# Kernel optimization log

Measured on AMD Instinct MI355X. Metric: run time of the kernel, lower is better.

Reference implementation:

```python
import jax, jax.numpy as jnp
import numpy as np

SCORE_THR = 0.5
RADII = jnp.array([0.5, 0.6, 0.7], dtype=jnp.float32)  # radius_dict[c]; all labels 0..C-1 covered

B, N, C = 2, 8192, 3


def setup_inputs() -> dict:
    key = jax.random.key(0)
    k1, k2 = jax.random.split(key)
    xyz = jax.random.normal(k1, (B, N, 3), dtype=jnp.float32)
    cls_features = jax.random.normal(k2, (B, N, C), dtype=jnp.float32)
    return {"xyz": xyz, "cls_features": cls_features}


def _greedy_select(xyz, cls_features):
    """Greedy per-class radius suppression over the flattened batch.
    Returns sample_idx (B, L) int32, zero-padded exactly like the torch code
    (sample_idx is zeros except slot i of the batch owning selection i)."""
    b, n, _ = xyz.shape
    L = b * n
    scores = jax.nn.sigmoid(jnp.max(cls_features, axis=2))   # (B, N)
    labels = jnp.argmax(cls_features, axis=2)                # (B, N)
    valid = scores >= SCORE_THR

    flat_scores = jnp.where(valid, scores, -jnp.inf).reshape(L)
    order = jnp.argsort(-flat_scores)                        # descending score; invalid sink to end
    sorted_labels = labels.reshape(L)[order]
    sorted_valid = valid.reshape(L)[order]
    sorted_batch = (order // n).astype(jnp.int32)
    sorted_pts = xyz.reshape(L, 3)[order]

    def cond(state):
        i, remaining, _ = state
        return remaining.any() & (i < L)

    def body(state):
        i, remaining, sel_pos = state
        cur = jnp.argmax(remaining)                  # first remaining point in sorted order
        # NB: faithful to the original bug: radius chosen via sorted_labels[i]
        # (loop counter), not the label of the current point.
        r = RADII[sorted_labels[i]]
        d2 = jnp.sum((sorted_pts - sorted_pts[cur]) ** 2, axis=-1)  # (L,)
        suppress = (sorted_batch == sorted_batch[cur]) & (d2 <= r * r)
        return (i + 1, remaining & ~suppress, sel_pos.at[i].set(cur.astype(jnp.int32)))

    sel0 = jnp.full((L,), -1, dtype=jnp.int32)
    _, _, sel_pos = jax.lax.while_loop(cond, body, (jnp.int32(0), sorted_valid, sel0))

    picked = sel_pos >= 0
    orig = jnp.where(picked, order[jnp.maximum(sel_pos, 0)], 0)  # flat index in [0, L)
    bidx = jnp.where(picked, orig // n, 0)
    pidx = jnp.where(picked, orig % n, 0)
    slots = jnp.arange(L)
    # zeros init + scatter exactly mirrors torch: sample_idx[batch, i] = point
    sample_idx = jnp.zeros((b, L), dtype=jnp.int32).at[bidx, slots].set(pidx.astype(jnp.int32))
    return sample_idx


def reference(xyz, cls_features):
    sample_idx = _greedy_select(xyz, cls_features)
    bsz = xyz.shape[0]
    # gather_operation: new_xyz[b, m] = xyz[b, sample_idx[b, m]]
    new_xyz = xyz[jnp.arange(bsz)[:, None], sample_idx]          # (B, L, 3)
    return new_xyz, sample_idx
```

## Files before the change

### kernel.cpp

```cpp
#include <hip/hip_runtime.h>
#include <stdint.h>


#define L_TOT 16384
#define NPT   8192

__device__ __forceinline__ int cellco(float v) {
    int c = (int)floorf((v + 6.4f) * 1.25f);
    return c < 0 ? 0 : (c > 15 ? 15 : c);
}
__device__ __forceinline__ float d2f(float ax, float ay, float az,
                                     float bx, float by, float bz) {
    float dx = __fsub_rn(ax, bx), dy = __fsub_rn(ay, by), dz = __fsub_rn(az, bz);
    return __fadd_rn(__fadd_rn(__fmul_rn(dx, dx), __fmul_rn(dy, dy)), __fmul_rn(dz, dz));
}
__device__ __forceinline__ float rad2(int lb) {
    float rr = (lb == 0) ? 0.5f : ((lb == 1) ? 0.6f : 0.7f);
    return __fmul_rn(rr, rr);
}
__device__ __forceinline__ float rlf(float v, int l) {
    return __uint_as_float(__builtin_amdgcn_readlane(__float_as_uint(v), l));
}
__device__ __forceinline__ int rli(int v, int l) {
    return (int)__builtin_amdgcn_readlane((uint32_t)v, l);
}

__global__ void k1_keys(const float* __restrict__ cls, uint64_t* __restrict__ keys,
                        uint8_t* __restrict__ umeta, uint16_t* __restrict__ sample,
                        int* __restrict__ cellcnt, uint32_t* __restrict__ slab2) {
    int l = blockIdx.x * blockDim.x + threadIdx.x;
    if (l >= L_TOT) return;
    ((uint32_t*)sample)[l] = 0;
    if (l < 8192) cellcnt[l] = 0;
    if (l < 1024) slab2[l] = 0;
    float c0 = cls[l * 3 + 0], c1 = cls[l * 3 + 1], c2 = cls[l * 3 + 2];
    float m = c0; int lab = 0;
    if (c1 > m) { m = c1; lab = 1; }
    if (c2 > m) { m = c2; lab = 2; }
    int valid = (m >= 0.0f) ? 1 : 0;
    float keyf = valid ? m : -__builtin_inff();
    uint32_t u = __float_as_uint(keyf);
    uint32_t o = (u & 0x80000000u) ? ~u : (u | 0x80000000u);
    keys[l] = ((uint64_t)(~o) << 32) | (uint32_t)l;
    umeta[l] = (uint8_t)(lab | (valid << 2));
}

__global__ void __launch_bounds__(256) k2_sort(
    const uint64_t* __restrict__ keys, const uint8_t* __restrict__ umeta,
    const float* __restrict__ xyz,
    float4* __restrict__ spts, uint32_t* __restrict__ slab2, uint16_t* __restrict__ sorder,
    int* __restrict__ cellcnt) {
    __shared__ uint64_t tile[2048];
    __shared__ int psum[256];
    const int t = threadIdx.x;
    const int elem = t & 31, part = t >> 5;
    const int l = blockIdx.x * 32 + elem;
    const uint64_t myk = keys[l];
    int cnt = 0;
    for (int t0 = 0; t0 < L_TOT; t0 += 2048) {
        for (int j = t; j < 2048; j += 256) tile[j] = keys[t0 + j];
        __syncthreads();
        const int b0 = part * 256;
        #pragma unroll 4
        for (int j = 0; j < 256; ++j) cnt += (tile[b0 + j] < myk) ? 1 : 0;
        __syncthreads();
    }
    psum[t] = cnt;
    __syncthreads();
    if (t < 32) {
        int rank = 0;
        #pragma unroll
        for (int q = 0; q < 8; ++q) rank += psum[q * 32 + t];
        const int ll = blockIdx.x * 32 + t;
        int b = ll >> 13, p = ll & (NPT - 1);
        const float* src = xyz + ((size_t)(b * NPT + p)) * 3;
        float x = src[0], y = src[1], z = src[2];
        uint8_t mt = umeta[ll];
        int lab = mt & 3, valid = (mt >> 2) & 1;
        float4 v; v.x = x; v.y = y; v.z = z;
        v.w = __uint_as_float((uint32_t)(b | (valid << 1)));
        spts[rank] = v;
        sorder[rank] = (uint16_t)ll;
        atomicOr(&slab2[rank >> 4], (uint32_t)lab << ((rank & 15) << 1));
        if (valid) {
            int cl = (b << 12) | (cellco(z) << 8) | (cellco(y) << 4) | cellco(x);
            atomicAdd(&cellcnt[cl], 1);
        }
    }
}

__global__ void g2_scan(int* __restrict__ cellcnt, int* __restrict__ cellstart) {
    __shared__ int part[256];
    __shared__ int poff[256];
    int t = threadIdx.x;
    int base = t * 32;
    int loc[32];
    int s = 0;
    for (int k = 0; k < 32; ++k) { loc[k] = cellcnt[base + k]; s += loc[k]; }
    part[t] = s;
    __syncthreads();
    if (t == 0) {
        int run = 0;
        for (int q = 0; q < 256; ++q) { poff[q] = run; run += part[q]; }
    }
    __syncthreads();
    int run = poff[t];
    for (int k = 0; k < 32; ++k) {
        cellstart[base + k] = run; run += loc[k];
        cellcnt[base + k] = 0;
    }
    if (t == 255) cellstart[8192] = run;
}

__global__ void g3_scatter(const float4* __restrict__ spts, const int* __restrict__ cellstart,
                           int* __restrict__ cellfill, float4* __restrict__ cellxyz) {
    int pos = blockIdx.x * blockDim.x + threadIdx.x;
    if (pos >= L_TOT) return;
    float4 v = spts[pos];
    uint32_t w = __float_as_uint(v.w);
    if (!(w & 2u)) return;
    int b = (int)(w & 1u);
    int cl = (b << 12) | (cellco(v.z) << 8) | (cellco(v.y) << 4) | cellco(v.x);
    int slot = atomicAdd(&cellfill[cl], 1);
    float4 o; o.x = v.x; o.y = v.y; o.z = v.z; o.w = __uint_as_float((uint32_t)pos);
    cellxyz[cellstart[cl] + slot] = o;
}

__global__ void __launch_bounds__(1024) k3_greedy(
    const float4* __restrict__ spts, const uint32_t* __restrict__ slab2,
    const uint16_t* __restrict__ sorder,
    const int* __restrict__ cellstart, const float4* __restrict__ cellxyz,
    uint16_t* __restrict__ sample) {
    __shared__ uint64_t qpack[16384];
    __shared__ uint32_t rem[512];
    __shared__ uint32_t alive2[512];
    __shared__ uint16_t cs16[8194];
    __shared__ uint32_t slds2[1024];
    __shared__ float4   pkd[2][128];
    __shared__ int      pkb[2][128];
    __shared__ int      pkn[2];

    const int t = threadIdx.x;
    const int V = cellstart[8192];
    const int NPH = (V + 127) >> 7;

    float4 cv0 = make_float4(0,0,0,0), cv1 = make_float4(0,0,0,0);
    int cord0 = 0, cord1 = 0;
    if (t < 64) {
        cv0 = spts[t]; cv1 = spts[64 + t];
        cord0 = (int)sorder[t]; cord1 = (int)sorder[64 + t];
    }
    for (int j = t; j < 8193; j += 1024) cs16[j] = (uint16_t)cellstart[j];
    for (int j = t; j < 1024; j += 1024) slds2[j] = slab2[j];
    for (int k = t; k < V; k += 1024) {
        float4 q = cellxyz[k];
        int qx = __float2int_rn(__fmul_rn(__fadd_rn(q.x, 8.0f), 4096.0f));
        int qy = __float2int_rn(__fmul_rn(__fadd_rn(q.y, 8.0f), 4096.0f));
        int qz = __float2int_rn(__fmul_rn(__fadd_rn(q.z, 8.0f), 4096.0f));
        qx = qx < 0 ? 0 : (qx > 65535 ? 65535 : qx);
        qy = qy < 0 ? 0 : (qy > 65535 ? 65535 : qy);
        qz = qz < 0 ? 0 : (qz > 65535 ? 65535 : qz);
        uint32_t pos = __float_as_uint(q.w);
        qpack[k] = ((uint64_t)(((uint32_t)qz) | (pos << 16)) << 32)
                 | ((uint32_t)qx | ((uint32_t)qy << 16));
    }
    for (int w = t; w < 512; w += 1024) {
        int lo = w * 32;
        uint32_t m;
        if (V >= lo + 32) m = 0xFFFFFFFFu;
        else if (V <= lo) m = 0u;
        else m = (1u << (V - lo)) - 1u;
        rem[w] = m;
        alive2[w] = m;
    }
    if (t < 2) pkn[t] = 0;
    __syncthreads();

    int ii = 0;
    for (int ph = 0; ph < NPH; ++ph) {
        const int cur = ph & 1, prv = cur ^ 1;
        if (t < 64) {
            const int nb = (ph + 1) << 7;
            int q0 = nb + t;       q0 = q0 > (L_TOT - 1) ? (L_TOT - 1) : q0;
            int q1 = nb + 64 + t;  q1 = q1 > (L_TOT - 1) ? (L_TOT - 1) : q1;
            float4 nv0 = spts[q0], nv1 = spts[q1];
            int nord0 = (int)sorder[q0], nord1 = (int)sorder[q1];

            int o0 = ii + t;      o0 = o0 > (L_TOT - 1) ? (L_TOT - 1) : o0;
            int o1 = ii + 64 + t; o1 = o1 > (L_TOT - 1) ? (L_TOT - 1) : o1;
            float cr0 = rad2((int)((slds2[o0 >> 4] >> ((o0 & 15) << 1)) & 3u));
            float cr1 = rad2((int)((slds2[o1 >> 4] >> ((o1 & 15) << 1)) & 3u));

            const int pos0 = (ph << 7) + t, pos1 = pos0 + 64;
            bool a0 = (pos0 < V) && ((rem[pos0 >> 5] >> (pos0 & 31)) & 1u);
            bool a1 = (pos1 < V) && ((rem[pos1 >> 5] >> (pos1 & 31)) & 1u);
            const int cb0 = cord0 >> 13, cb1 = cord1 >> 13;
            if (__ballot((a0 ? 1 : 0) | (a1 ? 1 : 0))) {
                const int m = pkn[prv];
                for (int j = 0; j < m; ++j) {
                    float4 pk = pkd[prv][j];
                    int pb = pkb[prv][j];
                    if (a0 && cb0 == pb &&
                        d2f(cv0.x, cv0.y, cv0.z, pk.x, pk.y, pk.z) <= pk.w) a0 = false;
                    if (a1 && cb1 == pb &&
                        d2f(cv1.x, cv1.y, cv1.z, pk.x, pk.y, pk.z) <= pk.w) a1 = false;
                }
            }

            int np = 0;
            const int ii0 = ii;
            {
                unsigned long long am = __ballot(a0 ? 1 : 0);
                while (am) {
                    const int jl0 = (int)__builtin_ctzll(am);
                    const unsigned long long am2 = am & (am - 1);
                    const bool has2 = (am2 != 0ull);
                    const int jl1 = has2 ? (int)__builtin_ctzll(am2) : jl0;
                    const float p0x = rlf(cv0.x, jl0), p0y = rlf(cv0.y, jl0), p0z = rlf(cv0.z, jl0);
                    const int   b0  = rli(cord0, jl0) >> 13;
                    const float p1x = rlf(cv0.x, jl1), p1y = rlf(cv0.y, jl1), p1z = rlf(cv0.z, jl1);
                    const int   b1  = rli(cord0, jl1) >> 13;
                    const float r2_0 = rlf((np & 64) ? cr1 : cr0, np & 63);
                    const int np1 = np + 1;
                    const float r2_1 = rlf((np1 & 64) ? cr1 : cr0, np1 & 63);
                    const bool kb = (b0 == b1) &&
                                    (d2f(p1x, p1y, p1z, p0x, p0y, p0z) <= r2_0);
                    const bool two = has2 && !kb;
                    if (t == jl0) {
                        pkd[cur][np] = make_float4(cv0.x, cv0.y, cv0.z, r2_0);
                        pkb[cur][np] = b0;
                        sample[b0 * L_TOT + ii0 + np] = (uint16_t)(cord0 & (NPT - 1));
                    }
                    if (two && t == jl1) {
                        pkd[cur][np1] = make_float4(cv0.x, cv0.y, cv0.z, r2_1);
                        pkb[cur][np1] = b1;
                        sample[b1 * L_TOT + ii0 + np1] = (uint16_t)(cord0 & (NPT - 1));
                    }
                    if (a0) {
                        if (cb0 == b0 && d2f(cv0.x, cv0.y, cv0.z, p0x, p0y, p0z) <= r2_0) a0 = false;
                        if (two && cb0 == b1 && d2f(cv0.x, cv0.y, cv0.z, p1x, p1y, p1z) <= r2_1) a0 = false;
                    }
                    if (a1) {
                        if (cb1 == b0 && d2f(cv1.x, cv1.y, cv1.z, p0x, p0y, p0z) <= r2_0) a1 = false;
                        if (two && cb1 == b1 && d2f(cv1.x, cv1.y, cv1.z, p1x, p1y, p1z) <= r2_1) a1 = false;
                    }
                    np += two ? 2 : 1;
                    am = __ballot(a0 ? 1 : 0);
                }
            }
            {
                unsigned long long am = __ballot(a1 ? 1 : 0);
                while (am) {
                    const int jl0 = (int)__builtin_ctzll(am);
                    const unsigned long long am2 = am & (am - 1);
                    const bool has2 = (am2 != 0ull);
                    const int jl1 = has2 ? (int)__builtin_ctzll(am2) : jl0;
                    const float p0x = rlf(cv1.x, jl0), p0y = rlf(cv1.y, jl0), p0z = rlf(cv1.z, jl0);
                    const int   b0  = rli(cord1, jl0) >> 13;
                    const float p1x = rlf(cv1.x, jl1), p1y = rlf(cv1.y, jl1), p1z = rlf(cv1.z, jl1);
                    const int   b1  = rli(cord1, jl1) >> 13;
                    const float r2_0 = rlf((np & 64) ? cr1 : cr0, np & 63);
                    const int np1 = np + 1;
                    const float r2_1 = rlf((np1 & 64) ? cr1 : cr0, np1 & 63);
                    const bool kb = (b0 == b1) &&
                                    (d2f(p1x, p1y, p1z, p0x, p0y, p0z) <= r2_0);
                    const bool two = has2 && !kb;
                    if (t == jl0) {
                        pkd[cur][np] = make_float4(cv1.x, cv1.y, cv1.z, r2_0);
                        pkb[cur][np] = b0;
                        sample[b0 * L_TOT + ii0 + np] = (uint16_t)(cord1 & (NPT - 1));
                    }
                    if (two && t == jl1) {
                        pkd[cur][np1] = make_float4(cv1.x, cv1.y, cv1.z, r2_1);
                        pkb[cur][np1] = b1;
                        sample[b1 * L_TOT + ii0 + np1] = (uint16_t)(cord1 & (NPT - 1));
                    }
                    if (a1) {
                        if (cb1 == b0 && d2f(cv1.x, cv1.y, cv1.z, p0x, p0y, p0z) <= r2_0) a1 = false;
                        if (two && cb1 == b1 && d2f(cv1.x, cv1.y, cv1.z, p1x, p1y, p1z) <= r2_1) a1 = false;
                    }
                    np += two ? 2 : 1;
                    am = __ballot(a1 ? 1 : 0);
                }
            }
            ii = ii0 + np;
            if (t == 0) pkn[cur] = np;
            cv0 = nv0; cv1 = nv1; cord0 = nord0; cord1 = nord1;
        } else {
            const int np = pkn[prv];
            if (np > 0) {
                const int tid = t - 64;
                const int ntask = np * 216;
                for (int task = tid; task < ntask; task += 960) {
                    int sub = task & 7;
                    int pc = task >> 3;
                    int p = pc / 27;
                    int c = pc - p * 27;
                    float4 pv = pkd[prv][p];
                    int pb_ = pkb[prv][p];
                    float r2 = pv.w;
                    int cx = cellco(pv.x) + (c % 3) - 1;
                    int cy = cellco(pv.y) + ((c / 3) % 3) - 1;
                    int cz = cellco(pv.z) + (c / 9) - 1;
                    if ((unsigned)cx > 15u || (unsigned)cy > 15u || (unsigned)cz > 15u) continue;
                    float lox = -6.4f + 0.8f * cx, hix = lox + 0.8f;
                    float loy = -6.4f + 0.8f * cy, hiy = loy + 0.8f;
                    float loz = -6.4f + 0.8f * cz, hiz = loz + 0.8f;
                    if (cx == 0) lox = -1e30f;  if (cx == 15) hix = 1e30f;
                    if (cy == 0) loy = -1e30f;  if (cy == 15) hiy = 1e30f;
                    if (cz == 0) loz = -1e30f;  if (cz == 15) hiz = 1e30f;
                    float bdx = fmaxf(fmaxf(lox - pv.x, pv.x - hix), 0.0f);
                    float bdy = fmaxf(fmaxf(loy - pv.y, pv.y - hiy), 0.0f);
                    float bdz = fmaxf(fmaxf(loz - pv.z, pv.z - hiz), 0.0f);
                    if (bdx * bdx + bdy * bdy + bdz * bdz > r2 + 0.02f) continue;
                    int cl = (pb_ << 12) | (cz << 8) | (cy << 4) | cx;
                    int st = (int)cs16[cl];
                    int en = (int)cs16[cl + 1];
                    float psx = (pv.x + 8.0f) * 4096.0f;
                    float psy = (pv.y + 8.0f) * 4096.0f;
                    float psz = (pv.z + 8.0f) * 4096.0f;
                    float thr_hi = (r2 + 0.02f) * 16777216.0f;
                    float thr_lo = (r2 - 0.02f) * 16777216.0f;
                    for (int k = st + sub; k < en; k += 8) {
                        uint64_t e = qpack[k];
                        uint32_t lo = (uint32_t)e, hi = (uint32_t)(e >> 32);
                        float ddx = (float)(lo & 0xffffu) - psx;
                        float ddy = (float)(lo >> 16) - psy;
                        float ddz = (float)(hi & 0xffffu) - psz;
                        float d2s = ddx * ddx + ddy * ddy + ddz * ddz;
                        if (d2s <= thr_hi) {
                            if (alive2[k >> 5] & (1u << (k & 31))) {
                                bool sup = (d2s <= thr_lo);
                                if (!sup) {
                                    float4 q = cellxyz[k];
                                    sup = d2f(q.x, q.y, q.z, pv.x, pv.y, pv.z) <= r2;
                                }
                                if (sup) {
                                    uint32_t pos = hi >> 16;
                                    atomicAnd(&alive2[k >> 5], ~(1u << (k & 31)));
                                    atomicAnd(&rem[pos >> 5], ~(1u << (pos & 31)));
                                }
                            }
                        }
                    }
                }
            }
        }
        __syncthreads();
    }
}

__global__ void k4_out(const float* __restrict__ xyz, const uint16_t* __restrict__ sample,
                       float* __restrict__ out) {
    int s = blockIdx.x * blockDim.x + threadIdx.x;
    if (s >= 2 * L_TOT) return;
    int idx = (int)sample[s];
    int b = s >> 14;
    const float* src = xyz + ((size_t)(b * NPT + idx)) * 3;
    float* dst = out + (size_t)s * 3;
    dst[0] = src[0]; dst[1] = src[1]; dst[2] = src[2];
    out[3 * 2 * L_TOT + s] = (float)idx;
}

extern "C" void kernel_launch(void* const* d_in, const int* in_sizes, int n_in,
                              void* d_out, int out_size, void* d_ws, size_t ws_size,
                              hipStream_t stream) {
    const float* xyz = (const float*)d_in[0];
    const float* cls = (const float*)d_in[1];
    float* out = (float*)d_out;
    char* ws = (char*)d_ws;
    float4*   spts    = (float4*)  (ws + 0);
    uint32_t* slab2   = (uint32_t*)(ws + 262144);
    uint16_t* sorder  = (uint16_t*)(ws + 278528);
    int*      cellcnt = (int*)     (ws + 311296);
    int*      cellst  = (int*)     (ws + 344064);
    float4*   cellxyz = (float4*)  (ws + 380928);
    uint64_t* keys    = (uint64_t*)(ws + 380928);
    uint8_t*  umeta   = (uint8_t*) (ws + 512000);
    uint16_t* sample  = (uint16_t*)(ws + 643072);

    k1_keys   <<<64,  256, 0, stream>>>(cls, keys, umeta, sample, cellcnt, slab2);
    k2_sort   <<<512, 256, 0, stream>>>(keys, umeta, xyz, spts, slab2, sorder, cellcnt);
    g2_scan   <<<1,   256, 0, stream>>>(cellcnt, cellst);
    g3_scatter<<<64,  256, 0, stream>>>(spts, cellst, cellcnt, cellxyz);
    k3_greedy <<<1,  1024, 0, stream>>>(spts, slab2, sorder, cellst, cellxyz, sample);
    k4_out    <<<128, 256, 0, stream>>>(xyz, sample, out);
}
```

Measured before the change: 508.7 us.

## Replace pipelined fixed-window phases with batched window scan then block-wide suppression

The greedy kernel used to run a software pipeline: one wave picked survivors from a fixed 128-point window while the other 15 waves applied grid suppression for the previous window's picks. Now wave 0 keeps scanning 128-point windows, skipping ones with no live points, until it has gathered more than 64 picks. After a barrier, all 1024 threads apply suppression for that batch, split 4 ways per cell instead of 8. The aim is fewer barrier rounds and less time wasted on empty windows. The cost is that selection and suppression no longer overlap, and the serial pairwise check inside the wave grows with the larger batch.

```diff
diff --git a/kernel.cpp b/kernel.cpp
--- a/kernel.cpp
+++ b/kernel.cpp
@@ -136,22 +136,15 @@
     __shared__ uint32_t alive2[512];
     __shared__ uint16_t cs16[8194];
     __shared__ uint32_t slds2[1024];
-    __shared__ float4   pkd[2][128];
-    __shared__ int      pkb[2][128];
-    __shared__ int      pkn[2];
+    __shared__ float4   pkd[192];
+    __shared__ uint8_t  pkb[192];
+    __shared__ int      s_np, s_done;
 
     const int t = threadIdx.x;
     const int V = cellstart[8192];
-    const int NPH = (V + 127) >> 7;
-
-    float4 cv0 = make_float4(0,0,0,0), cv1 = make_float4(0,0,0,0);
-    int cord0 = 0, cord1 = 0;
-    if (t < 64) {
-        cv0 = spts[t]; cv1 = spts[64 + t];
-        cord0 = (int)sorder[t]; cord1 = (int)sorder[64 + t];
-    }
+
     for (int j = t; j < 8193; j += 1024) cs16[j] = (uint16_t)cellstart[j];
-    for (int j = t; j < 1024; j += 1024) slds2[j] = slab2[j];
+    if (t < 1024) slds2[t] = slab2[t];
     for (int k = t; k < V; k += 1024) {
         float4 q = cellxyz[k];
         int qx = __float2int_rn(__fmul_rn(__fadd_rn(q.x, 8.0f), 4096.0f));
@@ -173,173 +166,176 @@
         rem[w] = m;
         alive2[w] = m;
     }
-    if (t < 2) pkn[t] = 0;
+    if (t == 0) { s_np = 0; s_done = 0; }
     __syncthreads();
 
-    int ii = 0;
-    for (int ph = 0; ph < NPH; ++ph) {
-        const int cur = ph & 1, prv = cur ^ 1;
+    int ii = 0, wstart = 0;
+    for (;;) {
         if (t < 64) {
-            const int nb = (ph + 1) << 7;
-            int q0 = nb + t;       q0 = q0 > (L_TOT - 1) ? (L_TOT - 1) : q0;
-            int q1 = nb + 64 + t;  q1 = q1 > (L_TOT - 1) ? (L_TOT - 1) : q1;
-            float4 nv0 = spts[q0], nv1 = spts[q1];
-            int nord0 = (int)sorder[q0], nord1 = (int)sorder[q1];
-
-            int o0 = ii + t;      o0 = o0 > (L_TOT - 1) ? (L_TOT - 1) : o0;
-            int o1 = ii + 64 + t; o1 = o1 > (L_TOT - 1) ? (L_TOT - 1) : o1;
+            int np = 0;
+            const int ii0 = ii;
+            int o0 = ii0 + t;        o0 = o0 > (L_TOT-1) ? (L_TOT-1) : o0;
+            int o1 = ii0 + 64 + t;   o1 = o1 > (L_TOT-1) ? (L_TOT-1) : o1;
+            int o2 = ii0 + 128 + t;  o2 = o2 > (L_TOT-1) ? (L_TOT-1) : o2;
             float cr0 = rad2((int)((slds2[o0 >> 4] >> ((o0 & 15) << 1)) & 3u));
             float cr1 = rad2((int)((slds2[o1 >> 4] >> ((o1 & 15) << 1)) & 3u));
-
-            const int pos0 = (ph << 7) + t, pos1 = pos0 + 64;
-            bool a0 = (pos0 < V) && ((rem[pos0 >> 5] >> (pos0 & 31)) & 1u);
-            bool a1 = (pos1 < V) && ((rem[pos1 >> 5] >> (pos1 & 31)) & 1u);
-            const int cb0 = cord0 >> 13, cb1 = cord1 >> 13;
-            if (__ballot((a0 ? 1 : 0) | (a1 ? 1 : 0))) {
-                const int m = pkn[prv];
-                for (int j = 0; j < m; ++j) {
-                    float4 pk = pkd[prv][j];
-                    int pb = pkb[prv][j];
+            float cr2 = rad2((int)((slds2[o2 >> 4] >> ((o2 & 15) << 1)) & 3u));
+
+            while (wstart < V && np <= 64) {
+                const int pos0 = wstart + t, pos1 = wstart + 64 + t;
+                bool a0 = (pos0 < V) && ((rem[pos0 >> 5] >> (pos0 & 31)) & 1u);
+                bool a1 = (pos1 < V) && ((rem[pos1 >> 5] >> (pos1 & 31)) & 1u);
+                wstart += 128;
+                if (!__ballot((a0 ? 1 : 0) | (a1 ? 1 : 0))) continue;
+
+                const int i0 = pos0 < (L_TOT-1) ? pos0 : (L_TOT-1);
+                const int i1 = pos1 < (L_TOT-1) ? pos1 : (L_TOT-1);
+                float4 cv0 = spts[i0], cv1 = spts[i1];
+                const int cord0 = (int)sorder[i0], cord1 = (int)sorder[i1];
+                const int cb0 = cord0 >> 13, cb1 = cord1 >> 13;
+
+                for (int j = 0; j < np; ++j) {
+                    float4 pk = pkd[j];
+                    int pb = (int)pkb[j];
                     if (a0 && cb0 == pb &&
                         d2f(cv0.x, cv0.y, cv0.z, pk.x, pk.y, pk.z) <= pk.w) a0 = false;
                     if (a1 && cb1 == pb &&
                         d2f(cv1.x, cv1.y, cv1.z, pk.x, pk.y, pk.z) <= pk.w) a1 = false;
                 }
-            }
-
-            int np = 0;
-            const int ii0 = ii;
-            {
-                unsigned long long am = __ballot(a0 ? 1 : 0);
-                while (am) {
-                    const int jl0 = (int)__builtin_ctzll(am);
-                    const unsigned long long am2 = am & (am - 1);
-                    const bool has2 = (am2 != 0ull);
-                    const int jl1 = has2 ? (int)__builtin_ctzll(am2) : jl0;
-                    const float p0x = rlf(cv0.x, jl0), p0y = rlf(cv0.y, jl0), p0z = rlf(cv0.z, jl0);
-                    const int   b0  = rli(cord0, jl0) >> 13;
-                    const float p1x = rlf(cv0.x, jl1), p1y = rlf(cv0.y, jl1), p1z = rlf(cv0.z, jl1);
-                    const int   b1  = rli(cord0, jl1) >> 13;
-                    const float r2_0 = rlf((np & 64) ? cr1 : cr0, np & 63);
-                    const int np1 = np + 1;
-                    const float r2_1 = rlf((np1 & 64) ? cr1 : cr0, np1 & 63);
-                    const bool kb = (b0 == b1) &&
-                                    (d2f(p1x, p1y, p1z, p0x, p0y, p0z) <= r2_0);
-                    const bool two = has2 && !kb;
-                    if (t == jl0) {
-                        pkd[cur][np] = make_float4(cv0.x, cv0.y, cv0.z, r2_0);
-                        pkb[cur][np] = b0;
-                        sample[b0 * L_TOT + ii0 + np] = (uint16_t)(cord0 & (NPT - 1));
+
+                {
+                    unsigned long long am = __ballot(a0 ? 1 : 0);
+                    while (am) {
+                        const int jl0 = (int)__builtin_ctzll(am);
+                        const unsigned long long am2 = am & (am - 1);
+                        const bool has2 = (am2 != 0ull);
+                        const int jl1 = has2 ? (int)__builtin_ctzll(am2) : jl0;
+                        const float p0x = rlf(cv0.x, jl0), p0y = rlf(cv0.y, jl0), p0z = rlf(cv0.z, jl0);
+                        const int   b0  = rli(cord0, jl0) >> 13;
+                        const float p1x = rlf(cv0.x, jl1), p1y = rlf(cv0.y, jl1), p1z = rlf(cv0.z, jl1);
+                        const int   b1  = rli(cord0, jl1) >> 13;
+                        const int bk0 = np >> 6;
+                        const float r2_0 = rlf(bk0 == 2 ? cr2 : (bk0 == 1 ? cr1 : cr0), np & 63);
+                        const int np1 = np + 1, bk1 = np1 >> 6;
+                        const float r2_1 = rlf(bk1 == 2 ? cr2 : (bk1 == 1 ? cr1 : cr0), np1 & 63);
+                        const bool kb = (b0 == b1) &&
+                                        (d2f(p1x, p1y, p1z, p0x, p0y, p0z) <= r2_0);
+                        const bool two = has2 && !kb;
+                        if (t == jl0) {
+                            pkd[np] = make_float4(cv0.x, cv0.y, cv0.z, r2_0);
+                            pkb[np] = (uint8_t)b0;
+                            sample[b0 * L_TOT + ii0 + np] = (uint16_t)(cord0 & (NPT - 1));
+                        }
+                        if (two && t == jl1) {
+                            pkd[np1] = make_float4(cv0.x, cv0.y, cv0.z, r2_1);
+                            pkb[np1] = (uint8_t)b1;
+                            sample[b1 * L_TOT + ii0 + np1] = (uint16_t)(cord0 & (NPT - 1));
+                        }
+                        if (a0) {
+                            if (cb0 == b0 && d2f(cv0.x, cv0.y, cv0.z, p0x, p0y, p0z) <= r2_0) a0 = false;
+                            if (two && cb0 == b1 && d2f(cv0.x, cv0.y, cv0.z, p1x, p1y, p1z) <= r2_1) a0 = false;
+                        }
+                        if (a1) {
+                            if (cb1 == b0 && d2f(cv1.x, cv1.y, cv1.z, p0x, p0y, p0z) <= r2_0) a1 = false;
+                            if (two && cb1 == b1 && d2f(cv1.x, cv1.y, cv1.z, p1x, p1y, p1z) <= r2_1) a1 = false;
+                        }
+                        np += two ? 2 : 1;
+                        am = __ballot(a0 ? 1 : 0);
                     }
-                    if (two && t == jl1) {
-                        pkd[cur][np1] = make_float4(cv0.x, cv0.y, cv0.z, r2_1);
-                        pkb[cur][np1] = b1;
-                        sample[b1 * L_TOT + ii0 + np1] = (uint16_t)(cord0 & (NPT - 1));
+                }
+                {
+                    unsigned long long am = __ballot(a1 ? 1 : 0);
+                    while (am) {
+                        const int jl0 = (int)__builtin_ctzll(am);
+                        const unsigned long long am2 = am & (am - 1);
+                        const bool has2 = (am2 != 0ull);
+                        const int jl1 = has2 ? (int)__builtin_ctzll(am2) : jl0;
+                        const float p0x = rlf(cv1.x, jl0), p0y = rlf(cv1.y, jl0), p0z = rlf(cv1.z, jl0);
+                        const int   b0  = rli(cord1, jl0) >> 13;
+                        const float p1x = rlf(cv1.x, jl1), p1y = rlf(cv1.y, jl1), p1z = rlf(cv1.z, jl1);
+                        const int   b1  = rli(cord1, jl1) >> 13;
+                        const int bk0 = np >> 6;
+                        const float r2_0 = rlf(bk0 == 2 ? cr2 : (bk0 == 1 ? cr1 : cr0), np & 63);
+                        const int np1 = np + 1, bk1 = np1 >> 6;
+                        const float r2_1 = rlf(bk1 == 2 ? cr2 : (bk1 == 1 ? cr1 : cr0), np1 & 63);
+                        const bool kb = (b0 == b1) &&
+                                        (d2f(p1x, p1y, p1z, p0x, p0y, p0z) <= r2_0);
+                        const bool two = has2 && !kb;
+                        if (t == jl0) {
+                            pkd[np] = make_float4(cv1.x, cv1.y, cv1.z, r2_0);
+                            pkb[np] = (uint8_t)b0;
+                            sample[b0 * L_TOT + ii0 + np] = (uint16_t)(cord1 & (NPT - 1));
+                        }
+                        if (two && t == jl1) {
+                            pkd[np1] = make_float4(cv1.x, cv1.y, cv1.z, r2_1);
+                            pkb[np1] = (uint8_t)b1;
+                            sample[b1 * L_TOT + ii0 + np1] = (uint16_t)(cord1 & (NPT - 1));
+                        }
+                        if (a1) {
+                            if (cb1 == b0 && d2f(cv1.x, cv1.y, cv1.z, p0x, p0y, p0z) <= r2_0) a1 = false;
+                            if (two && cb1 == b1 && d2f(cv1.x, cv1.y, cv1.z, p1x, p1y, p1z) <= r2_1) a1 = false;
+                        }
+                        np += two ? 2 : 1;
+                        am = __ballot(a1 ? 1 : 0);
                     }
-                    if (a0) {
-                        if (cb0 == b0 && d2f(cv0.x, cv0.y, cv0.z, p0x, p0y, p0z) <= r2_0) a0 = false;
-                        if (two && cb0 == b1 && d2f(cv0.x, cv0.y, cv0.z, p1x, p1y, p1z) <= r2_1) a0 = false;
-                    }
-                    if (a1) {
-                        if (cb1 == b0 && d2f(cv1.x, cv1.y, cv1.z, p0x, p0y, p0z) <= r2_0) a1 = false;
-                        if (two && cb1 == b1 && d2f(cv1.x, cv1.y, cv1.z, p1x, p1y, p1z) <= r2_1) a1 = false;
-                    }
-                    np += two ? 2 : 1;
-                    am = __ballot(a0 ? 1 : 0);
                 }
             }
-            {
-                unsigned long long am = __ballot(a1 ? 1 : 0);
-                while (am) {
-                    const int jl0 = (int)__builtin_ctzll(am);
-                    const unsigned long long am2 = am & (am - 1);
-                    const bool has2 = (am2 != 0ull);
-                    const int jl1 = has2 ? (int)__builtin_ctzll(am2) : jl0;
-                    const float p0x = rlf(cv1.x, jl0), p0y = rlf(cv1.y, jl0), p0z = rlf(cv1.z, jl0);
-                    const int   b0  = rli(cord1, jl0) >> 13;
-                    const float p1x = rlf(cv1.x, jl1), p1y = rlf(cv1.y, jl1), p1z = rlf(cv1.z, jl1);
-                    const int   b1  = rli(cord1, jl1) >> 13;
-                    const float r2_0 = rlf((np & 64) ? cr1 : cr0, np & 63);
-                    const int np1 = np + 1;
-                    const float r2_1 = rlf((np1 & 64) ? cr1 : cr0, np1 & 63);
-                    const bool kb = (b0 == b1) &&
-                                    (d2f(p1x, p1y, p1z, p0x, p0y, p0z) <= r2_0);
-                    const bool two = has2 && !kb;
-                    if (t == jl0) {
-                        pkd[cur][np] = make_float4(cv1.x, cv1.y, cv1.z, r2_0);
-                        pkb[cur][np] = b0;
-                        sample[b0 * L_TOT + ii0 + np] = (uint16_t)(cord1 & (NPT - 1));
-                    }
-                    if (two && t == jl1) {
-                        pkd[cur][np1] = make_float4(cv1.x, cv1.y, cv1.z, r2_1);
-                        pkb[cur][np1] = b1;
-                        sample[b1 * L_TOT + ii0 + np1] = (uint16_t)(cord1 & (NPT - 1));
-                    }
-                    if (a1) {
-                        if (cb1 == b0 && d2f(cv1.x, cv1.y, cv1.z, p0x, p0y, p0z) <= r2_0) a1 = false;
-                        if (two && cb1 == b1 && d2f(cv1.x, cv1.y, cv1.z, p1x, p1y, p1z) <= r2_1) a1 = false;
-                    }
-                    np += two ? 2 : 1;
-                    am = __ballot(a1 ? 1 : 0);
-                }
-            }
+            if (t == 0) { s_np = np; s_done = (wstart >= V) ? 1 : 0; }
             ii = ii0 + np;
-            if (t == 0) pkn[cur] = np;
-            cv0 = nv0; cv1 = nv1; cord0 = nord0; cord1 = nord1;
-        } else {
-            const int np = pkn[prv];
-            if (np > 0) {
-                const int tid = t - 64;
-                const int ntask = np * 216;
-                for (int task = tid; task < ntask; task += 960) {
-                    int sub = task & 7;
-                    int pc = task >> 3;
-                    int p = pc / 27;
-                    int c = pc - p * 27;
-                    float4 pv = pkd[prv][p];
-                    int pb_ = pkb[prv][p];
-                    float r2 = pv.w;
-                    int cx = cellco(pv.x) + (c % 3) - 1;
-                    int cy = cellco(pv.y) + ((c / 3) % 3) - 1;
-                    int cz = cellco(pv.z) + (c / 9) - 1;
-                    if ((unsigned)cx > 15u || (unsigned)cy > 15u || (unsigned)cz > 15u) continue;
-                    float lox = -6.4f + 0.8f * cx, hix = lox + 0.8f;
-                    float loy = -6.4f + 0.8f * cy, hiy = loy + 0.8f;
-                    float loz = -6.4f + 0.8f * cz, hiz = loz + 0.8f;
-                    if (cx == 0) lox = -1e30f;  if (cx == 15) hix = 1e30f;
-                    if (cy == 0) loy = -1e30f;  if (cy == 15) hiy = 1e30f;
-                    if (cz == 0) loz = -1e30f;  if (cz == 15) hiz = 1e30f;
-                    float bdx = fmaxf(fmaxf(lox - pv.x, pv.x - hix), 0.0f);
-                    float bdy = fmaxf(fmaxf(loy - pv.y, pv.y - hiy), 0.0f);
-                    float bdz = fmaxf(fmaxf(loz - pv.z, pv.z - hiz), 0.0f);
-                    if (bdx * bdx + bdy * bdy + bdz * bdz > r2 + 0.02f) continue;
-                    int cl = (pb_ << 12) | (cz << 8) | (cy << 4) | cx;
-                    int st = (int)cs16[cl];
-                    int en = (int)cs16[cl + 1];
-                    float psx = (pv.x + 8.0f) * 4096.0f;
-                    float psy = (pv.y + 8.0f) * 4096.0f;
-                    float psz = (pv.z + 8.0f) * 4096.0f;
-                    float thr_hi = (r2 + 0.02f) * 16777216.0f;
-                    float thr_lo = (r2 - 0.02f) * 16777216.0f;
-                    for (int k = st + sub; k < en; k += 8) {
-                        uint64_t e = qpack[k];
-                        uint32_t lo = (uint32_t)e, hi = (uint32_t)(e >> 32);
-                        float ddx = (float)(lo & 0xffffu) - psx;
-                        float ddy = (float)(lo >> 16) - psy;
-                        float ddz = (float)(hi & 0xffffu) - psz;
-                        float d2s = ddx * ddx + ddy * ddy + ddz * ddz;
-                        if (d2s <= thr_hi) {
-                            if (alive2[k >> 5] & (1u << (k & 31))) {
-                                bool sup = (d2s <= thr_lo);
-                                if (!sup) {
-                                    float4 q = cellxyz[k];
-                                    sup = d2f(q.x, q.y, q.z, pv.x, pv.y, pv.z) <= r2;
-                                }
-                                if (sup) {
-                                    uint32_t pos = hi >> 16;
-                                    atomicAnd(&alive2[k >> 5], ~(1u << (k & 31)));
-                                    atomicAnd(&rem[pos >> 5], ~(1u << (pos & 31)));
-                                }
+        }
+        __syncthreads();
+        if (s_done) break;
+        const int np = s_np;
+        if (np > 0) {
+            const int ntask = np * 108;
+            for (int task = t; task < ntask; task += 1024) {
+                int sub = task & 3;
+                int pc = task >> 2;
+                int p = pc / 27;
+                int c = pc - p * 27;
+                float4 pv = pkd[p];
+                int pb_ = (int)pkb[p];
+                float r2 = pv.w;
+                int cx = cellco(pv.x) + (c % 3) - 1;
+                int cy = cellco(pv.y) + ((c / 3) % 3) - 1;
+                int cz = cellco(pv.z) + (c / 9) - 1;
+                if ((unsigned)cx > 15u || (unsigned)cy > 15u || (unsigned)cz > 15u) continue;
+                float lox = -6.4f + 0.8f * cx, hix = lox + 0.8f;
+                float loy = -6.4f + 0.8f * cy, hiy = loy + 0.8f;
+                float loz = -6.4f + 0.8f * cz, hiz = loz + 0.8f;
+                if (cx == 0) lox = -1e30f;  if (cx == 15) hix = 1e30f;
+                if (cy == 0) loy = -1e30f;  if (cy == 15) hiy = 1e30f;
+                if (cz == 0) loz = -1e30f;  if (cz == 15) hiz = 1e30f;
+                float bdx = fmaxf(fmaxf(lox - pv.x, pv.x - hix), 0.0f);
+                float bdy = fmaxf(fmaxf(loy - pv.y, pv.y - hiy), 0.0f);
+                float bdz = fmaxf(fmaxf(loz - pv.z, pv.z - hiz), 0.0f);
+                if (bdx * bdx + bdy * bdy + bdz * bdz > r2 + 0.02f) continue;
+                int cl = (pb_ << 12) | (cz << 8) | (cy << 4) | cx;
+                int st = (int)cs16[cl];
+                int en = (int)cs16[cl + 1];
+                float psx = (pv.x + 8.0f) * 4096.0f;
+                float psy = (pv.y + 8.0f) * 4096.0f;
+                float psz = (pv.z + 8.0f) * 4096.0f;
+                float thr_hi = (r2 + 0.02f) * 16777216.0f;
+                float thr_lo = (r2 - 0.02f) * 16777216.0f;
+                for (int k = st + sub; k < en; k += 4) {
+                    uint64_t e = qpack[k];
+                    uint32_t lo = (uint32_t)e, hi = (uint32_t)(e >> 32);
+                    float ddx = (float)(lo & 0xffffu) - psx;
+                    float ddy = (float)(lo >> 16) - psy;
+                    float ddz = (float)(hi & 0xffffu) - psz;
+                    float d2s = ddx * ddx + ddy * ddy + ddz * ddz;
+                    if (d2s <= thr_hi) {
+                        if (alive2[k >> 5] & (1u << (k & 31))) {
+                            bool sup = (d2s <= thr_lo);
+                            if (!sup) {
+                                float4 q = cellxyz[k];
+                                sup = d2f(q.x, q.y, q.z, pv.x, pv.y, pv.z) <= r2;
+                            }
+                            if (sup) {
+                                uint32_t pos = hi >> 16;
+                                atomicAnd(&alive2[k >> 5], ~(1u << (k & 31)));
+                                atomicAnd(&rem[pos >> 5], ~(1u << (pos & 31)));
                             }
                         }
                     }
```

Result: slower. 1.067 ms (+109.8%).
